# Performance work log

Hardware: AMD Instinct MI355X
Metric: run time of the kernel (lower is better)

Reference implementation:

```python
import jax, jax.numpy as jnp
import numpy as np

B, S = 8192, 4096
EPS = 1e-6
ALPHA, BETA = 0.1, 0.1


def setup_inputs() -> dict:
    key = jax.random.key(0)
    k1, k2, k3, k4 = jax.random.split(key, 4)
    yhat = jax.random.normal(k1, (B, S), dtype=jnp.float32)
    y_dense = jax.random.normal(k2, (B, S), dtype=jnp.float32)
    keep = jax.random.bernoulli(k3, 0.5, (B, S))
    y = jnp.where(keep, y_dense, 0.0)
    # neighbor matrix: entries remapped {1.0->alpha, 2.0->beta}, mostly zero
    r = jax.random.randint(k4, (S, S), 0, 10)
    W = jnp.where(r == 1, ALPHA, jnp.where(r == 2, BETA, 0.0)).astype(jnp.float32)
    return {"yhat": yhat, "y": y, "W": W}


def reference(yhat, y, W):
    mask = (y != 0).astype(yhat.dtype)            # [B, S] nonzero-target mask
    sq = jnp.square(y - yhat)                      # [B, S] squared error
    # per-column loop `df_spatial_loss[:, i] = squared_error @ W[i]` == sq @ W.T
    spatial = sq @ W.T                             # [B, S] spatial regularization
    total = (sq + spatial) * mask                  # gather-at-nonzero == masking
    # mean over the nonzero entries only, then sqrt (RMSE)
    loss = jnp.sqrt(total.sum() / mask.sum() + EPS)
    return loss
```

## Files before the change

kernel.cpp:

```cpp
#include <hip/hip_runtime.h>
#include <math.h>

typedef unsigned long long u64;
typedef unsigned int u32;
typedef unsigned char u8;
typedef __attribute__((ext_vector_type(2))) unsigned long long u64x2;
typedef __attribute__((ext_vector_type(4))) int i32x4;

#define NB 8192
#define NS 4096

static const size_t OFF_CNT = 0;
static const size_t OFF_P3  = 16384;
static const size_t OFF_M8  = 32768;
static const size_t OFF_BT  = OFF_M8 + (size_t)NB * NS;
static const size_t WS_NEED = OFF_BT + (size_t)NS * NS;
static const size_t OFF_MB  = 32768;
static const size_t OFF_WB  = OFF_MB + (size_t)64 * NB * 8;

__device__ __forceinline__ void gload_lds16(const void* g, void* l) {
    __builtin_amdgcn_global_load_lds(
        (const __attribute__((address_space(1))) unsigned int*)g,
        (__attribute__((address_space(3))) unsigned int*)l, 16, 0, 0);
}


__global__ __launch_bounds__(256) void k12_prep(
    const float* __restrict__ y, const float* __restrict__ W,
    u32* __restrict__ m8, u32* __restrict__ bt, u64* __restrict__ pcnt)
{
    const int g = blockIdx.x;
    const int t = threadIdx.x;
    if (g < 2048) {
        __shared__ unsigned rc[4];
        const float4* y4 = (const float4*)y;
        size_t base = (size_t)g * 4096 + t;
        unsigned lcnt = 0;
        #pragma unroll 4
        for (int k = 0; k < 16; ++k) {
            float4 v = y4[base + (size_t)k * 256];
            unsigned b0 = v.x != 0.0f, b1 = v.y != 0.0f, b2 = v.z != 0.0f, b3 = v.w != 0.0f;
            lcnt += b0 + b1 + b2 + b3;
            m8[base + (size_t)k * 256] = b0 | (b1 << 8) | (b2 << 16) | (b3 << 24);
        }
        for (int off = 32; off; off >>= 1) lcnt += __shfl_down(lcnt, off, 64);
        if ((t & 63) == 0) rc[t >> 6] = lcnt;
        __syncthreads();
        if (t == 0) pcnt[g] = (u64)rc[0] + rc[1] + rc[2] + rc[3];
    } else {
        __shared__ float tile[64][65];
        const int gg = g - 2048;
        const int j0 = (gg & 63) * 64, i0 = (gg >> 6) * 64;
        #pragma unroll
        for (int k = 0; k < 16; ++k) {
            int lin = t + (k << 8);
            int r = lin >> 6, c = lin & 63;
            tile[r][c] = W[(size_t)(i0 + r) * NS + (j0 + c)];
        }
        __syncthreads();
        const int jj = t >> 2, ck = t & 3;
        u32 wd[4];
        #pragma unroll
        for (int gq = 0; gq < 4; ++gq) {
            u32 u = 0;
            #pragma unroll
            for (int bb = 0; bb < 4; ++bb)
                u |= (tile[ck * 16 + gq * 4 + bb][jj] != 0.0f ? 1u : 0u) << (8 * bb);
            wd[gq] = u;
        }
        uint4 out = make_uint4(wd[0], wd[1], wd[2], wd[3]);
        *(uint4*)&bt[(((size_t)(j0 + jj) << 12) + (size_t)(i0 + ck * 16)) >> 2] = out;
    }
}

__global__ __launch_bounds__(512, 2) void k3g_mfma(
    const float* __restrict__ y, const float* __restrict__ yhat,
    const u8* __restrict__ m8, const u8* __restrict__ bt,
    double* __restrict__ p3)
{
    __shared__ alignas(16) u8 lds[2][65536];
    const int b0 = blockIdx.x << 8;
    const int j0 = blockIdx.y << 8;
    const int t = threadIdx.x, l = t & 63, wv = t >> 6;
    const int wr = wv >> 2, wc = wv & 3;

    const int srow = t >> 3;
    const int schunk = (t & 7) ^ (srow & 7);
    const u8* sA = m8 + ((size_t)(b0 + srow) << 12) + ((size_t)schunk << 4);
    const u8* sB = bt + ((size_t)(j0 + srow) << 12) + ((size_t)schunk << 4);

    const int rl = l & 15, qh = l >> 4, rx = l & 7;
    const int sb0 = (((0 + qh) ^ rx) << 4);
    const int sb1 = (((4 + qh) ^ rx) << 4);

    i32x4 acc[8][4];
    #pragma unroll
    for (int i = 0; i < 8; ++i)
        #pragma unroll
        for (int j = 0; j < 4; ++j) acc[i][j] = (i32x4){0, 0, 0, 0};

    auto stage = [&](int kt2, int buf) {
        const size_t ko = (size_t)kt2 << 7;
        u8* dst = &lds[buf][0];
        #pragma unroll
        for (int h = 0; h < 2; ++h)
            #pragma unroll
            for (int c = 0; c < 2; ++c) {
                const size_t roff = ((size_t)(h * 128 + c * 64) << 12);
                u8* d = dst + h * 16384 + c * 8192 + (wv << 10);
                gload_lds16(sA + roff + ko, d);
                gload_lds16(sB + roff + ko, d + 32768);
            }
    };

    stage(0, 0);
    stage(1, 1);
    asm volatile("s_waitcnt vmcnt(8)" ::: "memory");
    __builtin_amdgcn_s_barrier();
    asm volatile("" ::: "memory");

    #pragma unroll 1
    for (int kt = 0; kt < 32; ++kt) {
        const u8* L = lds[kt & 1];

        i32x4 b[4][2];
        #pragma unroll
        for (int fc = 0; fc < 4; ++fc) {
            const int cbyte = 32768 + (((wc << 6) + (fc << 4) + rl) << 7);
            b[fc][0] = *(const i32x4*)&L[cbyte + sb0];
            b[fc][1] = *(const i32x4*)&L[cbyte + sb1];
        }
        #pragma unroll
        for (int q = 0; q < 4; ++q) {
            i32x4 a[2][2];
            #pragma unroll
            for (int i = 0; i < 2; ++i) {
                const int abyte = (((wr << 7) + ((2 * q + i) << 4) + rl) << 7);
                a[i][0] = *(const i32x4*)&L[abyte + sb0];
                a[i][1] = *(const i32x4*)&L[abyte + sb1];
            }
            __builtin_amdgcn_s_setprio(1);
            #pragma unroll
            for (int i = 0; i < 2; ++i)
                #pragma unroll
                for (int fc = 0; fc < 4; ++fc) {
                    acc[2 * q + i][fc] = __builtin_amdgcn_mfma_i32_16x16x64_i8(
                        a[i][0], b[fc][0], acc[2 * q + i][fc], 0, 0, 0);
                    acc[2 * q + i][fc] = __builtin_amdgcn_mfma_i32_16x16x64_i8(
                        a[i][1], b[fc][1], acc[2 * q + i][fc], 0, 0, 0);
                }
            __builtin_amdgcn_s_setprio(0);
        }

        if (kt < 31) {
            asm volatile("" ::: "memory");
            __builtin_amdgcn_s_barrier();
            asm volatile("" ::: "memory");
            if (kt < 30) {
                stage(kt + 2, kt & 1);
                asm volatile("s_waitcnt vmcnt(8)" ::: "memory");
            } else {
                asm volatile("s_waitcnt vmcnt(0)" ::: "memory");
            }
            __builtin_amdgcn_s_barrier();
            asm volatile("" ::: "memory");
        }
    }

    float part = 0.0f;
    const int col = j0 + (wc << 6) + rl;
    #pragma unroll
    for (int fr = 0; fr < 8; ++fr)
        #pragma unroll
        for (int q = 0; q < 4; ++q) {
            size_t rbase = ((size_t)(b0 + (wr << 7) + (fr << 4) + (qh << 2) + q) << 12) + col;
            #pragma unroll
            for (int fc = 0; fc < 4; ++fc) {
                float yv = y[rbase + (fc << 4)];
                float hv = yhat[rbase + (fc << 4)];
                float e = yv - hv;
                float wgt = 0.1f * (float)acc[fr][fc][q] + (yv != 0.0f ? 1.0f : 0.0f);
                part = fmaf(e * e, wgt, part);
            }
        }

    for (int off = 32; off; off >>= 1) part += __shfl_down(part, off, 64);
    float* red = (float*)lds;
    __syncthreads();
    if ((t & 63) == 0) red[t >> 6] = part;
    __syncthreads();
    if (t == 0) {
        float s = 0.0f;
        #pragma unroll
        for (int i = 0; i < 8; ++i) s += red[i];
        p3[(size_t)blockIdx.y * gridDim.x + blockIdx.x] = (double)s;
    }
}


__global__ __launch_bounds__(256) void k1_pack_mask(
    const float* __restrict__ y, u64* __restrict__ mbT, u64* __restrict__ pcnt)
{
    __shared__ unsigned rc[4];
    const unsigned t = threadIdx.x;
    const unsigned lane = t & 63;
    const float4* y4 = (const float4*)y;
    u64 qi = (u64)blockIdx.x * 256 + t;
    const u64 stride = (u64)2048 * 256;
    unsigned lcnt = 0;
    #pragma unroll 4
    for (int it = 0; it < 16; ++it, qi += stride) {
        float4 v = y4[qi];
        u64 b0 = __ballot(v.x != 0.0f);
        u64 b1 = __ballot(v.y != 0.0f);
        u64 b2 = __ballot(v.z != 0.0f);
        u64 b3 = __ballot(v.w != 0.0f);
        lcnt += (v.x != 0.0f) + (v.y != 0.0f) + (v.z != 0.0f) + (v.w != 0.0f);
        if (lane < 4) {
            unsigned sh = lane << 4;
            u64 word = ((b0 >> sh) & 0xFFFFull)
                     | (((b1 >> sh) & 0xFFFFull) << 16)
                     | (((b2 >> sh) & 0xFFFFull) << 32)
                     | (((b3 >> sh) & 0xFFFFull) << 48);
            u64 gw = ((qi - lane) >> 4) + lane;
            mbT[((gw & 63) << 13) + (gw >> 6)] = word;
        }
    }
    for (int off = 32; off; off >>= 1) lcnt += __shfl_down(lcnt, off, 64);
    if ((t & 63) == 0) rc[t >> 6] = lcnt;
    __syncthreads();
    if (t == 0) pcnt[blockIdx.x] = (u64)rc[0] + rc[1] + rc[2] + rc[3];
}

__global__ __launch_bounds__(256) void k2_pack_w(
    const float* __restrict__ W, u64* __restrict__ wbT)
{
    __shared__ float tile[64][65];
    const int j0 = blockIdx.x * 64;
    const int w  = blockIdx.y;
    const int i0 = w * 64;
    const int t = threadIdx.x;
    #pragma unroll
    for (int k = 0; k < 16; ++k) {
        int lin = t + (k << 8);
        int r = lin >> 6, c = lin & 63;
        tile[r][c] = W[(size_t)(i0 + r) * NS + (j0 + c)];
    }
    __syncthreads();
    const int lane = t & 63;
    const int wvv = t >> 6;
    const int pr = ((lane & 15) << 2) + (lane >> 4);
    for (int jj = wvv; jj < 64; jj += 4) {
        u64 bal = __ballot(tile[pr][jj] != 0.0f);
        if (lane == 0) wbT[((size_t)w << 12) + (j0 + jj)] = bal;
    }
}

__global__ __launch_bounds__(256) void k3_main(
    const float* __restrict__ y, const float* __restrict__ yhat,
    const u64* __restrict__ mbT, const u64* __restrict__ wbT,
    double* __restrict__ p3)
{
    __shared__ alignas(16) u64 mT[16 * 128];
    __shared__ alignas(16) u64 wT[16 * 128];
    const int b0 = blockIdx.x << 7;
    const int j0 = blockIdx.y << 7;
    const int t  = threadIdx.x;
    const int r0 = (t >> 4) << 3;
    const int cj = t & 15;
    const unsigned sx = ((unsigned)cj >> 2) << 4;

    unsigned cnt[8][8];
    #pragma unroll
    for (int a = 0; a < 8; ++a)
        #pragma unroll
        for (int b = 0; b < 8; ++b) cnt[a][b] = 0;

    char* mB = (char*)mT;
    char* wB = (char*)wT;

    #pragma unroll 1
    for (int s = 0; s < 4; ++s) {
        u64x2 gm[4], gq[4];
        #pragma unroll
        for (int k = 0; k < 4; ++k) {
            int lin = t + (k << 8);
            int wl = (s << 4) + (lin >> 6), c2 = lin & 63;
            gm[k] = *(const u64x2*)&mbT[((size_t)wl << 13) + b0 + 2 * c2];
            gq[k] = *(const u64x2*)&wbT[((size_t)wl << 12) + j0 + 2 * c2];
        }
        __syncthreads();
        #pragma unroll
        for (int k = 0; k < 4; ++k) {
            int lin = t + (k << 8);
            int wl = lin >> 6, c2 = lin & 63;
            int p = c2 ^ ((c2 >> 4) & 3);
            *(u64x2*)(mB + (wl << 10) + (c2 << 4)) = gm[k];
            *(u64x2*)(wB + (wl << 10) + (p << 4)) = gq[k];
        }
        __syncthreads();

        unsigned mo = (unsigned)(r0 << 3);
        unsigned qs = (unsigned)(cj << 6) + sx;
        #pragma unroll 2
        for (int w = 0; w < 16; ++w) {
            unsigned ml[16], ql[16];
            #pragma unroll
            for (int k = 0; k < 4; ++k) {
                uint4 a = *(const uint4*)(mB + mo + (k << 4));
                ml[4 * k + 0] = a.x; ml[4 * k + 1] = a.y;
                ml[4 * k + 2] = a.z; ml[4 * k + 3] = a.w;
                uint4 b = *(const uint4*)(wB + (qs ^ (unsigned)(k << 4)));
                ql[4 * k + 0] = b.x; ql[4 * k + 1] = b.y;
                ql[4 * k + 2] = b.z; ql[4 * k + 3] = b.w;
            }
            #pragma unroll
            for (int aa = 0; aa < 8; ++aa)
                #pragma unroll
                for (int bb = 0; bb < 8; ++bb) {
                    unsigned x0 = ml[2 * aa] & ql[2 * bb];
                    unsigned x1 = ml[2 * aa + 1] & ql[2 * bb + 1];
                    asm("v_bcnt_u32_b32 %0, %1, %0" : "+v"(cnt[aa][bb]) : "v"(x0));
                    asm("v_bcnt_u32_b32 %0, %1, %0" : "+v"(cnt[aa][bb]) : "v"(x1));
                }
            mo += 1024; qs += 1024;
        }
    }

    float part = 0.0f;
    const int c0 = cj << 3;
    #pragma unroll
    for (int aa = 0; aa < 8; ++aa) {
        size_t off = ((size_t)(b0 + r0 + aa) << 12) + (size_t)(j0 + c0);
        float ys[8], hs[8];
        *(float4*)&ys[0] = *(const float4*)(y + off);
        *(float4*)&ys[4] = *(const float4*)(y + off + 4);
        *(float4*)&hs[0] = *(const float4*)(yhat + off);
        *(float4*)&hs[4] = *(const float4*)(yhat + off + 4);
        #pragma unroll
        for (int bb = 0; bb < 8; ++bb) {
            float e = ys[bb] - hs[bb];
            float wgt = 0.1f * (float)cnt[aa][bb] + (ys[bb] != 0.0f ? 1.0f : 0.0f);
            part = fmaf(e * e, wgt, part);
        }
    }

    for (int off = 32; off; off >>= 1) part += __shfl_down(part, off, 64);
    float* red = (float*)mT;
    __syncthreads();
    if ((t & 63) == 0) red[t >> 6] = part;
    __syncthreads();
    if (t == 0)
        p3[(size_t)blockIdx.y * gridDim.x + blockIdx.x] =
            (double)red[0] + (double)red[1] + (double)red[2] + (double)red[3];
}

__global__ __launch_bounds__(256) void k4_final(
    const u64* __restrict__ pcnt, const double* __restrict__ p3, float* __restrict__ out,
    int np3)
{
    __shared__ double rs[4];
    __shared__ u64 rcc[4];
    double s3 = 0.0;
    u64 c = 0;
    for (int i = threadIdx.x; i < 2048; i += 256) c += pcnt[i];
    for (int i = threadIdx.x; i < np3; i += 256) s3 += p3[i];
    for (int off = 32; off; off >>= 1) {
        s3 += __shfl_down(s3, off, 64);
        c  += __shfl_down(c, off, 64);
    }
    int wv = threadIdx.x >> 6;
    if ((threadIdx.x & 63) == 0) { rs[wv] = s3; rcc[wv] = c; }
    __syncthreads();
    if (threadIdx.x == 0) {
        double S3 = rs[0] + rs[1] + rs[2] + rs[3];
        double C  = (double)(rcc[0] + rcc[1] + rcc[2] + rcc[3]);
        out[0] = (float)sqrt(S3 / C + 1e-6);
    }
}

extern "C" void kernel_launch(void* const* d_in, const int* in_sizes, int n_in,
                              void* d_out, int out_size, void* d_ws, size_t ws_size,
                              hipStream_t stream) {
    const float* yhat = (const float*)d_in[0];
    const float* y    = (const float*)d_in[1];
    const float* W    = (const float*)d_in[2];
    char* ws = (char*)d_ws;
    u64*    pcnt = (u64*)(ws + OFF_CNT);
    double* p3   = (double*)(ws + OFF_P3);

    if (ws_size >= WS_NEED) {
        u32* m8 = (u32*)(ws + OFF_M8);
        u32* bt = (u32*)(ws + OFF_BT);
        k12_prep<<<dim3(2048 + 4096), dim3(256), 0, stream>>>(y, W, m8, bt, pcnt);
        k3g_mfma<<<dim3(32, 16), dim3(512), 0, stream>>>(
            y, yhat, (const u8*)m8, (const u8*)bt, p3);
        k4_final<<<dim3(1), dim3(256), 0, stream>>>(pcnt, p3, (float*)d_out, 512);
    } else {
        u64* mbT = (u64*)(ws + OFF_MB);
        u64* wbT = (u64*)(ws + OFF_WB);
        k1_pack_mask<<<dim3(2048), dim3(256), 0, stream>>>(y, mbT, pcnt);
        k2_pack_w<<<dim3(64, 64), dim3(256), 0, stream>>>(W, wbT);
        k3_main<<<dim3(64, 32), dim3(256), 0, stream>>>(y, yhat, mbT, wbT, p3);
        k4_final<<<dim3(1), dim3(256), 0, stream>>>(pcnt, p3, (float*)d_out, 2048);
    }
}
```

Measured before the change: 200.2 us.

## Split LDS staging into per-half A/B tiles and interleave loads with MFMA

Reorganizes the LDS layout into separate half-tiles for A and B per buffer, and issues the global-to-LDS loads for the next stages inside the compute loop between MFMA groups instead of at a single point between two barriers. The A half-tiles for step m+1 are refilled once a mid-iteration barrier confirms the current A half has been consumed. B is prefetched two steps ahead. The goal is to overlap memory traffic with matrix math and cut barrier stalls. The cost is more intricate vmcnt and barrier accounting, where a wrong count would cause races.

```diff
diff --git a/kernel.cpp b/kernel.cpp
--- a/kernel.cpp
+++ b/kernel.cpp
@@ -78,7 +78,7 @@
     const u8* __restrict__ m8, const u8* __restrict__ bt,
     double* __restrict__ p3)
 {
-    __shared__ alignas(16) u8 lds[2][65536];
+    __shared__ alignas(16) u8 lds[131072];
     const int b0 = blockIdx.x << 8;
     const int j0 = blockIdx.y << 8;
     const int t = threadIdx.x, l = t & 63, wv = t >> 6;
@@ -86,12 +86,26 @@
 
     const int srow = t >> 3;
     const int schunk = (t & 7) ^ (srow & 7);
-    const u8* sA = m8 + ((size_t)(b0 + srow) << 12) + ((size_t)schunk << 4);
-    const u8* sB = bt + ((size_t)(j0 + srow) << 12) + ((size_t)schunk << 4);
+
+    auto stageA = [&](int kt, int h) {
+        const u8* src = m8 + ((size_t)(b0 + (h << 7) + srow) << 12)
+                        + (size_t)((kt << 7) + (schunk << 4));
+        u8* d = &lds[((((kt & 1) << 1) + h) << 14) + (wv << 10)];
+        gload_lds16(src, d);
+        gload_lds16(src + ((size_t)64 << 12), d + 8192);
+    };
+    auto stageB = [&](int kt, int h) {
+        const u8* src = bt + ((size_t)(j0 + (h << 7) + srow) << 12)
+                        + (size_t)((kt << 7) + (schunk << 4));
+        u8* d = &lds[65536 + ((((kt & 1) << 1) + h) << 14) + (wv << 10)];
+        gload_lds16(src, d);
+        gload_lds16(src + ((size_t)64 << 12), d + 8192);
+    };
 
     const int rl = l & 15, qh = l >> 4, rx = l & 7;
-    const int sb0 = (((0 + qh) ^ rx) << 4);
+    const int sb0 = ((qh ^ rx) << 4);
     const int sb1 = (((4 + qh) ^ rx) << 4);
+    const int bro = (wc & 1) << 6;
 
     i32x4 acc[8][4];
     #pragma unroll
@@ -99,45 +113,43 @@
         #pragma unroll
         for (int j = 0; j < 4; ++j) acc[i][j] = (i32x4){0, 0, 0, 0};
 
-    auto stage = [&](int kt2, int buf) {
-        const size_t ko = (size_t)kt2 << 7;
-        u8* dst = &lds[buf][0];
-        #pragma unroll
-        for (int h = 0; h < 2; ++h)
-            #pragma unroll
-            for (int c = 0; c < 2; ++c) {
-                const size_t roff = ((size_t)(h * 128 + c * 64) << 12);
-                u8* d = dst + h * 16384 + c * 8192 + (wv << 10);
-                gload_lds16(sA + roff + ko, d);
-                gload_lds16(sB + roff + ko, d + 32768);
+    stageA(0, 0); stageA(0, 1); stageB(0, 0); stageB(0, 1);
+    stageA(1, 0); stageA(1, 1); stageB(1, 0); stageB(1, 1);
+
+    #pragma unroll 1
+    for (int m = 0; m < 32; ++m) {
+        const int d = m & 1;
+        if (m == 0)       { asm volatile("s_waitcnt vmcnt(8)" ::: "memory"); }
+        else if (m == 31) { asm volatile("s_waitcnt vmcnt(0)" ::: "memory"); }
+        else              { asm volatile("s_waitcnt vmcnt(4)" ::: "memory"); }
+        __builtin_amdgcn_s_barrier();
+        asm volatile("" ::: "memory");
+
+        const u8* LA = &lds[(((d << 1) + wr) << 14)];
+        const u8* LB = &lds[65536 + (((d << 1) + (wc >> 1)) << 14)];
+
+        i32x4 b[4][2];
+        #pragma unroll
+        for (int q = 0; q < 4; ++q) {
+            if (q == 0) { if (m >= 1 && m <= 30) stageA(m + 1, 0); }
+            else if (q == 1) { if (m >= 1 && m <= 30) stageA(m + 1, 1); }
+            else if (q == 2) { if (m <= 29) stageB(m + 2, 0); }
+            else             { if (m <= 29) stageB(m + 2, 1); }
+
+            if (q == 0) {
+                #pragma unroll
+                for (int fc = 0; fc < 4; ++fc) {
+                    const int lr = bro + (fc << 4) + rl;
+                    b[fc][0] = *(const i32x4*)&LB[(lr << 7) + sb0];
+                    b[fc][1] = *(const i32x4*)&LB[(lr << 7) + sb1];
+                }
             }
-    };
-
-    stage(0, 0);
-    stage(1, 1);
-    asm volatile("s_waitcnt vmcnt(8)" ::: "memory");
-    __builtin_amdgcn_s_barrier();
-    asm volatile("" ::: "memory");
-
-    #pragma unroll 1
-    for (int kt = 0; kt < 32; ++kt) {
-        const u8* L = lds[kt & 1];
-
-        i32x4 b[4][2];
-        #pragma unroll
-        for (int fc = 0; fc < 4; ++fc) {
-            const int cbyte = 32768 + (((wc << 6) + (fc << 4) + rl) << 7);
-            b[fc][0] = *(const i32x4*)&L[cbyte + sb0];
-            b[fc][1] = *(const i32x4*)&L[cbyte + sb1];
-        }
-        #pragma unroll
-        for (int q = 0; q < 4; ++q) {
             i32x4 a[2][2];
             #pragma unroll
             for (int i = 0; i < 2; ++i) {
-                const int abyte = (((wr << 7) + ((2 * q + i) << 4) + rl) << 7);
-                a[i][0] = *(const i32x4*)&L[abyte + sb0];
-                a[i][1] = *(const i32x4*)&L[abyte + sb1];
+                const int lr = (((q << 1) + i) << 4) + rl;
+                a[i][0] = *(const i32x4*)&LA[(lr << 7) + sb0];
+                a[i][1] = *(const i32x4*)&LA[(lr << 7) + sb1];
             }
             __builtin_amdgcn_s_setprio(1);
             #pragma unroll
@@ -150,20 +162,12 @@
                         a[i][1], b[fc][1], acc[2 * q + i][fc], 0, 0, 0);
                 }
             __builtin_amdgcn_s_setprio(0);
-        }
-
-        if (kt < 31) {
-            asm volatile("" ::: "memory");
-            __builtin_amdgcn_s_barrier();
-            asm volatile("" ::: "memory");
-            if (kt < 30) {
-                stage(kt + 2, kt & 1);
-                asm volatile("s_waitcnt vmcnt(8)" ::: "memory");
-            } else {
-                asm volatile("s_waitcnt vmcnt(0)" ::: "memory");
+
+            if (q == 0) {
+                asm volatile("" ::: "memory");
+                __builtin_amdgcn_s_barrier();
+                asm volatile("" ::: "memory");
             }
-            __builtin_amdgcn_s_barrier();
-            asm volatile("" ::: "memory");
         }
     }
 
```

Result: faster. 190.9 us (-4.6%).
